# Kernel tuning notes

Hardware: AMD Instinct MI355X
Metric: run time of the kernel (lower is better)

## Reference

```python
import jax, jax.numpy as jnp
import numpy as np

BL = 512  # block length (self.bl)

def _conv1x1(x, W, b):
    # x: [B, Cin, L], W: [Cout, Cin], b: [Cout]
    return jnp.einsum('bcl,oc->bol', x, W) + b[None, :, None]


def setup_inputs() -> dict:
    key = jax.random.key(0)
    ks = jax.random.split(key, 10)
    B, L = 4, 8192
    q_dim = k_dim = v_dim = 512
    c = q_dim // 2  # r1=r2=r3=2 -> 256
    s = 0.05
    return {
        'x1': jax.random.normal(ks[0], (B, q_dim, L), jnp.float32),
        'mask': jnp.ones((B, 1, L), jnp.float32),
        'Wq': jax.random.normal(ks[1], (c, q_dim), jnp.float32) * s,
        'bq': jnp.zeros((c,), jnp.float32),
        'Wk': jax.random.normal(ks[2], (c, k_dim), jnp.float32) * s,
        'bk': jnp.zeros((c,), jnp.float32),
        'Wv': jax.random.normal(ks[3], (c, v_dim), jnp.float32) * s,
        'bv': jnp.zeros((c,), jnp.float32),
        'Wo': jax.random.normal(ks[4], (v_dim, c), jnp.float32) * s,
        'bo': jnp.zeros((v_dim,), jnp.float32),
    }


def _sliding_att(q, k, v, mask):
    B, c1, L = q.shape
    c3 = v.shape[1]
    nb = L // BL
    half = BL // 2
    ws = BL + 2 * half  # window size
    # queries per block: [B*nb, c1, BL]
    qb = q.reshape(B, c1, nb, BL).transpose(0, 2, 1, 3).reshape(B * nb, c1, BL)
    # overlapping k/v/mask windows via gather (unfold equivalent)
    idx = jnp.arange(nb)[:, None] * BL + jnp.arange(ws)[None, :]  # [nb, ws]
    def windows(t, C):
        tp = jnp.pad(t, ((0, 0), (0, 0), (half, half)))
        tw = tp[:, :, idx]                       # [B, C, nb, ws]
        return tw.transpose(0, 2, 1, 3).reshape(B * nb, C, ws)
    kb = windows(k, c1)
    vb = windows(v, c3)
    mb = windows(mask, 1)                        # [B*nb, 1, ws]
    energy = jnp.einsum('mcq,mck->mqk', qb, kb) / jnp.sqrt(jnp.float32(c1))
    energy = energy + jnp.log(mb + 1e-6)         # mb broadcasts over q dim
    att = jax.nn.softmax(energy, axis=-1) * mb   # [B*nb, BL, ws]
    out = jnp.einsum('mck,mqk->mcq', vb, att)    # [B*nb, c3, BL]
    return out, nb


def reference(x1, mask, Wq, bq, Wk, bk, Wv, bv, Wo, bo):
    q = _conv1x1(x1, Wq, bq)
    k = _conv1x1(x1, Wk, bk)
    v = _conv1x1(x1, Wv, bv)   # encoder: value from x1
    B, _, L = q.shape
    out, nb = _sliding_att(q, k, v, mask)
    out = _conv1x1(jax.nn.relu(out), Wo, bo)     # [B*nb, v_dim, BL]
    v_dim = Wo.shape[0]
    out = out.reshape(B, nb, v_dim, BL).transpose(0, 2, 1, 3).reshape(B, v_dim, L)
    return out * mask[:, 0:1, :]
```

## Files before the change

### kernel.cpp

```cpp
#include <hip/hip_runtime.h>

typedef short short8 __attribute__((ext_vector_type(8)));
typedef float f32x4 __attribute__((ext_vector_type(4)));
typedef unsigned short ushort4v __attribute__((ext_vector_type(4)));

#define MFMA(a, b, c) __builtin_amdgcn_mfma_f32_16x16x32_bf16((a), (b), (c), 0, 0, 0)

__device__ __forceinline__ short f2bf(float f) {
  union { float f; unsigned u; } v; v.f = f;
  unsigned r = v.u + 0x7fffu + ((v.u >> 16) & 1u);
  return (short)(r >> 16);
}

__device__ __forceinline__ void glds16(const short* g, short* l) {
  __builtin_amdgcn_global_load_lds((const __attribute__((address_space(1))) void*)g,
                                   (__attribute__((address_space(3))) void*)l, 16, 0, 0);
}

__global__ __launch_bounds__(256) void convert_w(
    const float* __restrict__ Wq, const float* __restrict__ Wk,
    const float* __restrict__ Wv, const float* __restrict__ Wo,
    const float* __restrict__ bq, const float* __restrict__ bk,
    const float* __restrict__ bv,
    short* __restrict__ Wb3, short* __restrict__ Wob, float* __restrict__ b3) {
  int idx = blockIdx.x * 256 + threadIdx.x;
  const int NW3 = 768 * 512, NWO = 512 * 256;
  if (idx < NW3) {
    int o = idx >> 9, cix = idx & 511;
    const float* W = (o < 256) ? Wq : (o < 512) ? Wk : Wv;
    Wb3[idx] = f2bf(W[(o & 255) * 512 + cix]);
  } else if (idx < NW3 + NWO) {
    int i2 = idx - NW3;
    Wob[i2] = f2bf(Wo[i2]);
  } else if (idx < NW3 + NWO + 768) {
    int i3 = idx - (NW3 + NWO);
    b3[i3] = (i3 < 256) ? bq[i3] : (i3 < 512) ? bk[i3 - 256] : bv[i3 - 512];
  }
}

__global__ __launch_bounds__(256) void transpose_x(const float* __restrict__ x,
                                                   short* __restrict__ xT) {
  __shared__ float t[64][65];
  int b = blockIdx.z, c0 = blockIdx.y * 64, l0 = blockIdx.x * 64;
  int tid = threadIdx.x;
  {
    int cl = tid >> 2, ls = (tid & 3) * 16;
    const float* xb = x + ((size_t)b * 512 + c0 + cl) * 8192 + l0 + ls;
#pragma unroll
    for (int i = 0; i < 4; i++) {
      f32x4 v = *(const f32x4*)(xb + i * 4);
      *(f32x4*)&t[cl][ls + i * 4] = v;
    }
  }
  __syncthreads();
  {
    int ll = tid >> 2, cs = (tid & 3) * 16;
    short8 pk[2];
#pragma unroll
    for (int h = 0; h < 2; h++)
#pragma unroll
      for (int j = 0; j < 8; j++) pk[h][j] = f2bf(t[cs + h * 8 + j][ll]);
    short* xo = xT + ((size_t)b * 8192 + l0 + ll) * 512 + c0 + cs;
    *(short8*)(xo) = pk[0];
    *(short8*)(xo + 8) = pk[1];
  }
}

__global__ __launch_bounds__(256, 2) void gemm_qkv(
    const short* __restrict__ Wb3, const float* __restrict__ b3,
    const short* __restrict__ xT, short* __restrict__ q_t,
    short* __restrict__ k_t, short* __restrict__ v_tt) {
  __shared__ __align__(16) short lds[8192];
  int t = threadIdx.x, w = t >> 6, l = t & 63;
  int r = l & 15, g = l >> 4;
  int wr = w >> 1, wc = w & 1;
  int id = blockIdx.x;
  int xcd = id & 7, j = id >> 3;
  int grp = j / 6, mtile = j - 6 * grp;
  int g_total = xcd * 32 + grp;
  int n0 = (g_total >> 2) * 128, b = g_total & 3;
  int m00 = mtile * 128;
  const short* Ab = Wb3 + (size_t)m00 * 512;
  const short* Bb = xT + (size_t)b * 8192 * 512 + (size_t)n0 * 512;
  int c0 = w * 64 + l, c1 = 256 + w * 64 + l;
  int a0r = c0 >> 2, a0c = (c0 & 3) * 8, a1r = c1 >> 2, a1c = (c1 & 3) * 8;

  f32x4 acc[4][4];
#pragma unroll
  for (int i = 0; i < 4; i++)
#pragma unroll
    for (int jj = 0; jj < 4; jj++) acc[i][jj] = {0.f, 0.f, 0.f, 0.f};

  for (int kk = 0; kk < 16; kk++) {
    const short* ga = Ab + kk * 32;
    const short* gb = Bb + kk * 32;
    glds16(ga + (size_t)a0r * 512 + a0c, lds + (w * 64) * 8);
    glds16(ga + (size_t)a1r * 512 + a1c, lds + (256 + w * 64) * 8);
    glds16(gb + (size_t)a0r * 512 + a0c, lds + 4096 + (w * 64) * 8);
    glds16(gb + (size_t)a1r * 512 + a1c, lds + 4096 + (256 + w * 64) * 8);
    __syncthreads();
    short8 af[4], bfv[4];
#pragma unroll
    for (int mt = 0; mt < 4; mt++)
      af[mt] = *(const short8*)(lds + (wr * 64 + mt * 16 + r) * 32 + g * 8);
#pragma unroll
    for (int nt = 0; nt < 4; nt++)
      bfv[nt] = *(const short8*)(lds + 4096 + (wc * 64 + nt * 16 + r) * 32 + g * 8);
#pragma unroll
    for (int mt = 0; mt < 4; mt++)
#pragma unroll
      for (int nt = 0; nt < 4; nt++) acc[mt][nt] = MFMA(af[mt], bfv[nt], acc[mt][nt]);
    __syncthreads();
  }

  if (mtile < 4) {
    short* dst = ((mtile < 2) ? q_t : k_t) + (size_t)b * 8192 * 256;
    int cb = (mtile & 1) * 128 + wr * 64;
#pragma unroll
    for (int nt = 0; nt < 4; nt++) {
      int n = n0 + wc * 64 + nt * 16 + r;
#pragma unroll
      for (int mt = 0; mt < 4; mt++) {
        ushort4v pk;
#pragma unroll
        for (int jj = 0; jj < 4; jj++)
          pk[jj] = (unsigned short)f2bf(acc[mt][nt][jj] + b3[m00 + wr * 64 + mt * 16 + 4 * g + jj]);
        *(ushort4v*)(dst + (size_t)n * 256 + cb + mt * 16 + 4 * g) = pk;
      }
    }
  } else {
    short* dst = v_tt + (size_t)b * 256 * 8192;
    int cb = (mtile - 4) * 128 + wr * 64;
#pragma unroll
    for (int mt = 0; mt < 4; mt++)
#pragma unroll
      for (int jj = 0; jj < 4; jj++) {
        int c = cb + mt * 16 + 4 * g + jj;
        float bias = b3[512 + c];
#pragma unroll
        for (int nt = 0; nt < 4; nt++)
          dst[(size_t)c * 8192 + n0 + wc * 64 + nt * 16 + r] = f2bf(acc[mt][nt][jj] + bias);
      }
  }
}

__global__ __launch_bounds__(256, 2) void attn(
    const short* __restrict__ q_t, const short* __restrict__ k_t,
    const short* __restrict__ v_tt, const float* __restrict__ mask,
    short* __restrict__ attout) {
  __shared__ __align__(16) short kv[37376];
  int t = threadIdx.x;
  int lane = t & 63, w = t >> 6;
  int r = lane & 15, g = lane >> 4;
  int id = blockIdx.x;
  int xcd = id & 7, m8 = id >> 3;
  int qtile = m8 & 7;
  int grp = ((m8 >> 3) << 3) + xcd;
  int blk = grp & 15, b = grp >> 4;
  const short* qtb = q_t + (size_t)b * 8192 * 256;
  const short* ktb = k_t + (size_t)b * 8192 * 256;
  const short* vtb = v_tt + (size_t)b * 256 * 8192;
  const float* mrow = mask + (size_t)b * 8192;
  int q0 = blk * 512 + qtile * 64 + w * 16;
  short* plds_w = kv + 32768 + w * 1152;

  short8 qf[8];
#pragma unroll
  for (int cc = 0; cc < 8; cc++)
    qf[cc] = *(const short8*)(qtb + (size_t)(q0 + r) * 256 + cc * 32 + g * 8);

  f32x4 zero = {0.f, 0.f, 0.f, 0.f};
  short8 zero8 = {0, 0, 0, 0, 0, 0, 0, 0};
  f32x4 o[16];
#pragma unroll
  for (int i = 0; i < 16; i++) o[i] = zero;
  float m_run[4] = {-1e30f, -1e30f, -1e30f, -1e30f};
  float lsum[4] = {0.f, 0.f, 0.f, 0.f};
  int wbase = blk * 512 - 256;

  short8 kreg[8], vreg[8];
  auto ld_chunk = [&](int kbase) {
#pragma unroll
    for (int i = 0; i < 8; i++) {
      int s = t + i * 256;
      int row = s >> 5, sl = s & 31;
      int kg = kbase + row;
      kreg[i] = zero8;
      if (kg >= 0 && kg < 8192) kreg[i] = *(const short8*)(ktb + (size_t)kg * 256 + sl * 8);
    }
#pragma unroll
    for (int i = 0; i < 8; i++) {
      int s = t + i * 256;
      int chn = s >> 3, sl = s & 7;
      int kg = kbase + sl * 8;
      vreg[i] = zero8;
      if (kg >= 0 && kg <= 8192 - 8) vreg[i] = *(const short8*)(vtb + (size_t)chn * 8192 + kg);
    }
  };
  auto st_chunk = [&]() {
#pragma unroll
    for (int i = 0; i < 8; i++) {
      int s = t + i * 256;
      int row = s >> 5, sl = s & 31;
      *(short8*)(kv + row * 256 + ((sl ^ (row & 7)) * 8)) = kreg[i];
    }
#pragma unroll
    for (int i = 0; i < 8; i++) {
      int s = t + i * 256;
      int chn = s >> 3, sl = s & 7;
      *(short8*)(kv + 16384 + chn * 64 + ((sl ^ (chn & 7)) * 8)) = vreg[i];
    }
  };

  ld_chunk(wbase);

  for (int ch = 0; ch < 16; ch++) {
    int kbase = wbase + ch * 64;
    st_chunk();
    __syncthreads();
    if (ch < 15) ld_chunk(kbase + 64);

    f32x4 e[4];
    float lm[4], mvv[4];
    __builtin_amdgcn_s_setprio(1);
#pragma unroll
    for (int kt = 0; kt < 4; kt++) {
      e[kt] = zero;
      int kg = kbase + kt * 16 + r;
      bool val = (kg >= 0) && (kg < 8192);
      float mv = val ? mrow[kg] : 0.f;
      mvv[kt] = mv;
      lm[kt] = __logf(mv + 1e-6f);
      const short* kr = kv + (kt * 16 + r) * 256;
#pragma unroll
      for (int cc = 0; cc < 8; cc++) {
        short8 kf = *(const short8*)(kr + (((cc * 4 + g) ^ (r & 7)) * 8));
        e[kt] = MFMA(qf[cc], kf, e[kt]);
      }
    }
    __builtin_amdgcn_s_setprio(0);
#pragma unroll
    for (int kt = 0; kt < 4; kt++)
#pragma unroll
      for (int j = 0; j < 4; j++) e[kt][j] = e[kt][j] * 0.0625f + lm[kt];
    float mx[4];
#pragma unroll
    for (int j = 0; j < 4; j++)
      mx[j] = fmaxf(fmaxf(e[0][j], e[1][j]), fmaxf(e[2][j], e[3][j]));
#pragma unroll
    for (int d = 1; d < 16; d <<= 1)
#pragma unroll
      for (int j = 0; j < 4; j++) mx[j] = fmaxf(mx[j], __shfl_xor(mx[j], d));
    float need = 0.f;
#pragma unroll
    for (int j = 0; j < 4; j++) need = fmaxf(need, mx[j] - m_run[j]);
    if (!__all(need <= 8.f)) {
      float scl[4];
#pragma unroll
      for (int j = 0; j < 4; j++) {
        float mn = fmaxf(m_run[j], mx[j]);
        scl[j] = __expf(m_run[j] - mn);
        m_run[j] = mn;
        lsum[j] *= scl[j];
      }
#pragma unroll
      for (int ct = 0; ct < 16; ct++)
#pragma unroll
        for (int j = 0; j < 4; j++) o[ct][j] *= scl[j];
    }
#pragma unroll
    for (int kt = 0; kt < 4; kt++)
#pragma unroll
      for (int j = 0; j < 4; j++) {
        float p = __expf(e[kt][j] - m_run[j]);
        lsum[j] += p;
        e[kt][j] = p * mvv[kt];
      }

#pragma unroll
    for (int kt = 0; kt < 4; kt++)
#pragma unroll
      for (int j = 0; j < 4; j++)
        plds_w[(4 * g + j) * 72 + kt * 16 + r] = f2bf(e[kt][j]);

    __builtin_amdgcn_s_setprio(1);
#pragma unroll
    for (int ks = 0; ks < 2; ks++) {
      short8 pa = *(const short8*)(plds_w + r * 72 + ks * 32 + g * 8);
#pragma unroll
      for (int ct = 0; ct < 16; ct++) {
        short8 vf = *(const short8*)(kv + 16384 + (ct * 16 + r) * 64 +
                                     (((ks * 4 + g) ^ (r & 7)) * 8));
        o[ct] = MFMA(pa, vf, o[ct]);
      }
    }
    __builtin_amdgcn_s_setprio(0);
    if (ch < 15) __syncthreads();
  }
#pragma unroll
  for (int d = 1; d < 16; d <<= 1)
#pragma unroll
    for (int j = 0; j < 4; j++) lsum[j] += __shfl_xor(lsum[j], d);
  float inv[4];
#pragma unroll
  for (int j = 0; j < 4; j++) inv[j] = 1.0f / lsum[j];
  short* ao = attout + (size_t)b * 8192 * 256;
#pragma unroll
  for (int ct = 0; ct < 16; ct++)
#pragma unroll
    for (int j = 0; j < 4; j++) {
      float vv = fmaxf(o[ct][j] * inv[j], 0.f);
      ao[(size_t)(q0 + 4 * g + j) * 256 + ct * 16 + r] = f2bf(vv);
    }
}

__global__ __launch_bounds__(256, 2) void gemm_out(
    const short* __restrict__ Wob, const float* __restrict__ bo,
    const short* __restrict__ attout, const float* __restrict__ mask,
    float* __restrict__ out) {
  __shared__ __align__(16) short lds[8192];
  int t = threadIdx.x, w = t >> 6, l = t & 63;
  int r = l & 15, g = l >> 4;
  int wr = w >> 1, wc = w & 1;
  int id = blockIdx.x;
  int xcd = id & 7, j = id >> 3;
  int grp = j >> 2, member = j & 3;
  int g_total = xcd * 32 + grp;
  int n0 = (g_total >> 2) * 128, b = g_total & 3;
  int m00 = member * 128;
  const short* Ab = Wob + (size_t)m00 * 256;
  const short* Bb = attout + (size_t)b * 8192 * 256 + (size_t)n0 * 256;
  int c0 = w * 64 + l, c1 = 256 + w * 64 + l;
  int a0r = c0 >> 2, a0c = (c0 & 3) * 8, a1r = c1 >> 2, a1c = (c1 & 3) * 8;

  f32x4 acc[4][4];
#pragma unroll
  for (int i = 0; i < 4; i++)
#pragma unroll
    for (int jj = 0; jj < 4; jj++) acc[i][jj] = {0.f, 0.f, 0.f, 0.f};

  for (int kk = 0; kk < 8; kk++) {
    const short* ga = Ab + kk * 32;
    const short* gb = Bb + kk * 32;
    glds16(ga + (size_t)a0r * 256 + a0c, lds + (w * 64) * 8);
    glds16(ga + (size_t)a1r * 256 + a1c, lds + (256 + w * 64) * 8);
    glds16(gb + (size_t)a0r * 256 + a0c, lds + 4096 + (w * 64) * 8);
    glds16(gb + (size_t)a1r * 256 + a1c, lds + 4096 + (256 + w * 64) * 8);
    __syncthreads();
    short8 af[4], bfv[4];
#pragma unroll
    for (int mt = 0; mt < 4; mt++)
      af[mt] = *(const short8*)(lds + (wr * 64 + mt * 16 + r) * 32 + g * 8);
#pragma unroll
    for (int nt = 0; nt < 4; nt++)
      bfv[nt] = *(const short8*)(lds + 4096 + (wc * 64 + nt * 16 + r) * 32 + g * 8);
#pragma unroll
    for (int mt = 0; mt < 4; mt++)
#pragma unroll
      for (int nt = 0; nt < 4; nt++) acc[mt][nt] = MFMA(af[mt], bfv[nt], acc[mt][nt]);
    __syncthreads();
  }

  float* ob = out + (size_t)b * 512 * 8192;
#pragma unroll
  for (int nt = 0; nt < 4; nt++) {
    int n = n0 + wc * 64 + nt * 16 + r;
    float mv = mask[(size_t)b * 8192 + n];
#pragma unroll
    for (int mt = 0; mt < 4; mt++)
#pragma unroll
      for (int jj = 0; jj < 4; jj++) {
        int m = m00 + wr * 64 + mt * 16 + 4 * g + jj;
        ob[(size_t)m * 8192 + n] = (acc[mt][nt][jj] + bo[m]) * mv;
      }
  }
}

extern "C" void kernel_launch(void* const* d_in, const int* in_sizes, int n_in,
                              void* d_out, int out_size, void* d_ws, size_t ws_size,
                              hipStream_t stream) {
  const float* x1 = (const float*)d_in[0];
  const float* mask = (const float*)d_in[1];
  const float* Wq = (const float*)d_in[2];
  const float* bq = (const float*)d_in[3];
  const float* Wk = (const float*)d_in[4];
  const float* bk = (const float*)d_in[5];
  const float* Wv = (const float*)d_in[6];
  const float* bv = (const float*)d_in[7];
  const float* Wo = (const float*)d_in[8];
  const float* bo = (const float*)d_in[9];

  char* ws = (char*)d_ws;
  size_t off = 0;
  short* xT = (short*)(ws + off);  off += (size_t)4 * 8192 * 512 * 2;
  short* q_t = (short*)(ws + off); off += (size_t)4 * 8192 * 256 * 2;
  short* k_t = (short*)(ws + off); off += (size_t)4 * 8192 * 256 * 2;
  short* v_tt = (short*)(ws + off); off += (size_t)4 * 8192 * 256 * 2;
  short* aout = (short*)(ws + off); off += (size_t)4 * 8192 * 256 * 2;
  short* Wb3 = (short*)(ws + off); off += 768 * 512 * 2;
  short* Wob = (short*)(ws + off); off += 512 * 256 * 2;
  float* b3 = (float*)(ws + off);  off += 768 * 4;

  convert_w<<<dim3(2051), dim3(256), 0, stream>>>(Wq, Wk, Wv, Wo, bq, bk, bv, Wb3, Wob, b3);
  transpose_x<<<dim3(128, 8, 4), dim3(256), 0, stream>>>(x1, xT);
  gemm_qkv<<<dim3(1536), dim3(256), 0, stream>>>(Wb3, b3, xT, q_t, k_t, v_tt);
  attn<<<dim3(512), dim3(256), 0, stream>>>(q_t, k_t, v_tt, mask, aout);
  gemm_out<<<dim3(1024), dim3(256), 0, stream>>>(Wob, bo, aout, mask, (float*)d_out);
}
```

Baseline: 297.0 us.

## Double-buffer GEMM LDS staging and prefetch mask in attention pipeline

```diff
diff --git a/kernel.cpp b/kernel.cpp
--- a/kernel.cpp
+++ b/kernel.cpp
@@ -70,7 +70,7 @@
     const short* __restrict__ Wb3, const float* __restrict__ b3,
     const short* __restrict__ xT, short* __restrict__ q_t,
     short* __restrict__ k_t, short* __restrict__ v_tt) {
-  __shared__ __align__(16) short lds[8192];
+  __shared__ __align__(16) short lds[16384];
   int t = threadIdx.x, w = t >> 6, l = t & 63;
   int r = l & 15, g = l >> 4;
   int wr = w >> 1, wc = w & 1;
@@ -85,32 +85,41 @@
   int c0 = w * 64 + l, c1 = 256 + w * 64 + l;
   int a0r = c0 >> 2, a0c = (c0 & 3) * 8, a1r = c1 >> 2, a1c = (c1 & 3) * 8;
 
-  f32x4 acc[4][4];
-#pragma unroll
-  for (int i = 0; i < 4; i++)
-#pragma unroll
-    for (int jj = 0; jj < 4; jj++) acc[i][jj] = {0.f, 0.f, 0.f, 0.f};
-
-  for (int kk = 0; kk < 16; kk++) {
+  auto STAGE = [&](int buf, int kk) {
     const short* ga = Ab + kk * 32;
     const short* gb = Bb + kk * 32;
-    glds16(ga + (size_t)a0r * 512 + a0c, lds + (w * 64) * 8);
-    glds16(ga + (size_t)a1r * 512 + a1c, lds + (256 + w * 64) * 8);
-    glds16(gb + (size_t)a0r * 512 + a0c, lds + 4096 + (w * 64) * 8);
-    glds16(gb + (size_t)a1r * 512 + a1c, lds + 4096 + (256 + w * 64) * 8);
-    __syncthreads();
+    short* lb = lds + buf * 8192;
+    glds16(ga + (size_t)a0r * 512 + a0c, lb + (w * 64) * 8);
+    glds16(ga + (size_t)a1r * 512 + a1c, lb + (256 + w * 64) * 8);
+    glds16(gb + (size_t)a0r * 512 + a0c, lb + 4096 + (w * 64) * 8);
+    glds16(gb + (size_t)a1r * 512 + a1c, lb + 4096 + (256 + w * 64) * 8);
+  };
+
+  f32x4 acc[4][4];
+#pragma unroll
+  for (int i = 0; i < 4; i++)
+#pragma unroll
+    for (int jj = 0; jj < 4; jj++) acc[i][jj] = {0.f, 0.f, 0.f, 0.f};
+
+  STAGE(0, 0);
+  __syncthreads();
+  int cur = 0;
+  for (int kk = 0; kk < 16; kk++) {
+    if (kk + 1 < 16) STAGE(cur ^ 1, kk + 1);
+    const short* lb = lds + cur * 8192;
     short8 af[4], bfv[4];
 #pragma unroll
     for (int mt = 0; mt < 4; mt++)
-      af[mt] = *(const short8*)(lds + (wr * 64 + mt * 16 + r) * 32 + g * 8);
+      af[mt] = *(const short8*)(lb + (wr * 64 + mt * 16 + r) * 32 + g * 8);
 #pragma unroll
     for (int nt = 0; nt < 4; nt++)
-      bfv[nt] = *(const short8*)(lds + 4096 + (wc * 64 + nt * 16 + r) * 32 + g * 8);
+      bfv[nt] = *(const short8*)(lb + 4096 + (wc * 64 + nt * 16 + r) * 32 + g * 8);
 #pragma unroll
     for (int mt = 0; mt < 4; mt++)
 #pragma unroll
       for (int nt = 0; nt < 4; nt++) acc[mt][nt] = MFMA(af[mt], bfv[nt], acc[mt][nt]);
     __syncthreads();
+    cur ^= 1;
   }
 
   if (mtile < 4) {
@@ -179,6 +188,7 @@
   int wbase = blk * 512 - 256;
 
   short8 kreg[8], vreg[8];
+  float mreg[4];
   auto ld_chunk = [&](int kbase) {
 #pragma unroll
     for (int i = 0; i < 8; i++) {
@@ -196,6 +206,11 @@
       vreg[i] = zero8;
       if (kg >= 0 && kg <= 8192 - 8) vreg[i] = *(const short8*)(vtb + (size_t)chn * 8192 + kg);
     }
+#pragma unroll
+    for (int kt = 0; kt < 4; kt++) {
+      int kg = kbase + kt * 16 + r;
+      mreg[kt] = (kg >= 0 && kg < 8192) ? mrow[kg] : 0.f;
+    }
   };
   auto st_chunk = [&]() {
 #pragma unroll
@@ -216,21 +231,21 @@
 
   for (int ch = 0; ch < 16; ch++) {
     int kbase = wbase + ch * 64;
+    float mvv[4];
+#pragma unroll
+    for (int kt = 0; kt < 4; kt++) mvv[kt] = mreg[kt];
     st_chunk();
-    __syncthreads();
+    asm volatile("s_waitcnt lgkmcnt(0)" ::: "memory");
+    __builtin_amdgcn_s_barrier();
     if (ch < 15) ld_chunk(kbase + 64);
+    __builtin_amdgcn_sched_barrier(0);
 
     f32x4 e[4];
-    float lm[4], mvv[4];
-    __builtin_amdgcn_s_setprio(1);
+    float lm[4];
 #pragma unroll
     for (int kt = 0; kt < 4; kt++) {
       e[kt] = zero;
-      int kg = kbase + kt * 16 + r;
-      bool val = (kg >= 0) && (kg < 8192);
-      float mv = val ? mrow[kg] : 0.f;
-      mvv[kt] = mv;
-      lm[kt] = __logf(mv + 1e-6f);
+      lm[kt] = __logf(mvv[kt] + 1e-6f);
       const short* kr = kv + (kt * 16 + r) * 256;
 #pragma unroll
       for (int cc = 0; cc < 8; cc++) {
@@ -238,7 +253,6 @@
         e[kt] = MFMA(qf[cc], kf, e[kt]);
       }
     }
-    __builtin_amdgcn_s_setprio(0);
 #pragma unroll
     for (int kt = 0; kt < 4; kt++)
 #pragma unroll
@@ -283,7 +297,6 @@
       for (int j = 0; j < 4; j++)
         plds_w[(4 * g + j) * 72 + kt * 16 + r] = f2bf(e[kt][j]);
 
-    __builtin_amdgcn_s_setprio(1);
 #pragma unroll
     for (int ks = 0; ks < 2; ks++) {
       short8 pa = *(const short8*)(plds_w + r * 72 + ks * 32 + g * 8);
@@ -294,8 +307,10 @@
         o[ct] = MFMA(pa, vf, o[ct]);
       }
     }
-    __builtin_amdgcn_s_setprio(0);
-    if (ch < 15) __syncthreads();
+    if (ch < 15) {
+      asm volatile("s_waitcnt lgkmcnt(0)" ::: "memory");
+      __builtin_amdgcn_s_barrier();
+    }
   }
 #pragma unroll
   for (int d = 1; d < 16; d <<= 1)
@@ -318,7 +333,7 @@
     const short* __restrict__ Wob, const float* __restrict__ bo,
     const short* __restrict__ attout, const float* __restrict__ mask,
     float* __restrict__ out) {
-  __shared__ __align__(16) short lds[8192];
+  __shared__ __align__(16) short lds[16384];
   int t = threadIdx.x, w = t >> 6, l = t & 63;
   int r = l & 15, g = l >> 4;
   int wr = w >> 1, wc = w & 1;
@@ -333,32 +348,41 @@
   int c0 = w * 64 + l, c1 = 256 + w * 64 + l;
   int a0r = c0 >> 2, a0c = (c0 & 3) * 8, a1r = c1 >> 2, a1c = (c1 & 3) * 8;
 
-  f32x4 acc[4][4];
-#pragma unroll
-  for (int i = 0; i < 4; i++)
-#pragma unroll
-    for (int jj = 0; jj < 4; jj++) acc[i][jj] = {0.f, 0.f, 0.f, 0.f};
-
-  for (int kk = 0; kk < 8; kk++) {
+  auto STAGE = [&](int buf, int kk) {
     const short* ga = Ab + kk * 32;
     const short* gb = Bb + kk * 32;
-    glds16(ga + (size_t)a0r * 256 + a0c, lds + (w * 64) * 8);
-    glds16(ga + (size_t)a1r * 256 + a1c, lds + (256 + w * 64) * 8);
-    glds16(gb + (size_t)a0r * 256 + a0c, lds + 4096 + (w * 64) * 8);
-    glds16(gb + (size_t)a1r * 256 + a1c, lds + 4096 + (256 + w * 64) * 8);
-    __syncthreads();
+    short* lb = lds + buf * 8192;
+    glds16(ga + (size_t)a0r * 256 + a0c, lb + (w * 64) * 8);
+    glds16(ga + (size_t)a1r * 256 + a1c, lb + (256 + w * 64) * 8);
+    glds16(gb + (size_t)a0r * 256 + a0c, lb + 4096 + (w * 64) * 8);
+    glds16(gb + (size_t)a1r * 256 + a1c, lb + 4096 + (256 + w * 64) * 8);
+  };
+
+  f32x4 acc[4][4];
+#pragma unroll
+  for (int i = 0; i < 4; i++)
+#pragma unroll
+    for (int jj = 0; jj < 4; jj++) acc[i][jj] = {0.f, 0.f, 0.f, 0.f};
+
+  STAGE(0, 0);
+  __syncthreads();
+  int cur = 0;
+  for (int kk = 0; kk < 8; kk++) {
+    if (kk + 1 < 8) STAGE(cur ^ 1, kk + 1);
+    const short* lb = lds + cur * 8192;
     short8 af[4], bfv[4];
 #pragma unroll
     for (int mt = 0; mt < 4; mt++)
-      af[mt] = *(const short8*)(lds + (wr * 64 + mt * 16 + r) * 32 + g * 8);
+      af[mt] = *(const short8*)(lb + (wr * 64 + mt * 16 + r) * 32 + g * 8);
 #pragma unroll
     for (int nt = 0; nt < 4; nt++)
-      bfv[nt] = *(const short8*)(lds + 4096 + (wc * 64 + nt * 16 + r) * 32 + g * 8);
+      bfv[nt] = *(const short8*)(lb + 4096 + (wc * 64 + nt * 16 + r) * 32 + g * 8);
 #pragma unroll
     for (int mt = 0; mt < 4; mt++)
 #pragma unroll
       for (int nt = 0; nt < 4; nt++) acc[mt][nt] = MFMA(af[mt], bfv[nt], acc[mt][nt]);
     __syncthreads();
+    cur ^= 1;
   }
 
   float* ob = out + (size_t)b * 512 * 8192;
```

New measurement: 311.8 us. 5.0% more time.
